# Optimization experiments

Hardware: AMD Instinct MI355X
Metric: run time of the kernel (lower is better)

The kernel has to match this reference:

```python
import jax, jax.numpy as jnp
import numpy as np

N, K, FN, O = 2048, 8, 16, 32


def setup_inputs() -> dict:
    key = jax.random.key(0)
    k1, k2, k3, k4 = jax.random.split(key, 4)
    node_features = jax.random.normal(k1, (N, FN), dtype=jnp.float32)
    edge_feat_matrix = jax.random.normal(k2, (N, N, K), dtype=jnp.float32)
    adj_matrix = jax.random.uniform(k3, (N, N), dtype=jnp.float32)
    stdv = 1.0 / np.sqrt(O)
    weight = jax.random.uniform(k4, (K + FN, O), dtype=jnp.float32,
                                minval=-stdv, maxval=stdv)
    return {"node_features": node_features,
            "edge_feat_matrix": edge_feat_matrix,
            "adj_matrix": adj_matrix,
            "weight": weight}


def reference(node_features, edge_feat_matrix, adj_matrix, weight):
    # Row-normalize adjacency: D^{-1} A (tensor_normalize in __init__)
    row_sum = adj_matrix.sum(axis=1)
    r_inv = jnp.where(jnp.isfinite(1.0 / row_sum), 1.0 / row_sum, 0.0)
    adj = r_inv[:, None] * adj_matrix  # [N, N]

    # Original math: combined[i,j] = cat(edge[i,j], x[j]); support = combined @ W
    # out[j,o] = sum_i adj[i,j] * support[i,j,o]
    # Split W so we never materialize the [N,N,K+FN] or [N,N,O] tensors.
    k = edge_feat_matrix.shape[-1]
    W_e, W_n = weight[:k], weight[k:]
    agg_e = jnp.einsum('ij,ijk->jk', adj, edge_feat_matrix)  # [N, K]
    col_sum = adj.sum(axis=0)                                 # [N]
    out = agg_e @ W_e + col_sum[:, None] * (node_features @ W_n)  # [N, O]
    return out
```

## Files before the change

### kernel.cpp

```cpp
#include <hip/hip_runtime.h>
#include <hip/hip_bf16.h>

constexpr int CN  = 2048;
constexpr int CK  = 8;
constexpr int CFN = 16;
constexpr int CO  = 32;

constexpr int JTILE  = 256;
constexpr int NJT    = CN / JTILE;
constexpr int CHUNK  = 32;
constexpr int NCHUNK = CN / CHUNK;

__global__ __launch_bounds__(256) void rowsum_k(const float* __restrict__ adj,
                                                float* __restrict__ rinv) {
    const int i = blockIdx.x;
    const int t = threadIdx.x;
    const float4* row = (const float4*)(adj + (size_t)i * CN);
    float4 v0 = row[t], v1 = row[t + 256];
    float s = v0.x + v0.y + v0.z + v0.w + v1.x + v1.y + v1.z + v1.w;
    #pragma unroll
    for (int off = 32; off > 0; off >>= 1) s += __shfl_down(s, off, 64);
    __shared__ float partial[4];
    if ((t & 63) == 0) partial[t >> 6] = s;
    __syncthreads();
    if (t == 0) {
        float tot = partial[0] + partial[1] + partial[2] + partial[3];
        float r = 1.0f / tot;
        if (!isfinite(r)) r = 0.0f;
        rinv[i] = r;
    }
}

__global__ __launch_bounds__(256) void main_k(const float* __restrict__ E,
                                              const float* __restrict__ adj,
                                              const float* __restrict__ rinv,
                                              float* __restrict__ agg,
                                              float* __restrict__ col) {
    const int j  = blockIdx.x * JTILE + threadIdx.x;
    const int i0 = blockIdx.y * CHUNK;

    float acc[CK];
    #pragma unroll
    for (int k = 0; k < CK; ++k) acc[k] = 0.f;
    float colacc = 0.f;

    #pragma unroll 4
    for (int ii = 0; ii < CHUNK; ++ii) {
        const int i = i0 + ii;
        const float a = rinv[i] * adj[(size_t)i * CN + j];
        const float4* ev = (const float4*)(E + ((size_t)i * CN + j) * CK);
        const float4 e0 = ev[0];
        const float4 e1 = ev[1];
        acc[0] += a * e0.x; acc[1] += a * e0.y;
        acc[2] += a * e0.z; acc[3] += a * e0.w;
        acc[4] += a * e1.x; acc[5] += a * e1.y;
        acc[6] += a * e1.z; acc[7] += a * e1.w;
        colacc += a;
    }

    float* aj = agg + (size_t)j * CK;
    #pragma unroll
    for (int k = 0; k < CK; ++k) atomicAdd(aj + k, acc[k]);
    atomicAdd(col + j, colacc);
}

__global__ __launch_bounds__(256) void epilogue_k(const float* __restrict__ agg,
                                                  const float* __restrict__ col,
                                                  const float* __restrict__ nf,
                                                  const float* __restrict__ wt,
                                                  float* __restrict__ out) {
    const int gid = blockIdx.x * 256 + threadIdx.x;
    const int j = gid >> 5;
    const int o = gid & 31;
    float s1 = 0.f;
    #pragma unroll
    for (int k = 0; k < CK; ++k)
        s1 += agg[(size_t)j * CK + k] * wt[k * CO + o];
    float s2 = 0.f;
    #pragma unroll
    for (int f = 0; f < CFN; ++f)
        s2 += nf[(size_t)j * CFN + f] * wt[(CK + f) * CO + o];
    out[gid] = s1 + col[j] * s2;
}

extern "C" void kernel_launch(void* const* d_in, const int* in_sizes, int n_in,
                              void* d_out, int out_size, void* d_ws, size_t ws_size,
                              hipStream_t stream) {
    const float *nf = nullptr, *E = nullptr, *adj = nullptr, *wt = nullptr;
    for (int i = 0; i < n_in; ++i) {
        switch (in_sizes[i]) {
            case CN * CFN:        nf  = (const float*)d_in[i]; break;
            case CN * CN * CK:    E   = (const float*)d_in[i]; break;
            case CN * CN:         adj = (const float*)d_in[i]; break;
            case (CK + CFN) * CO: wt  = (const float*)d_in[i]; break;
        }
    }
    float* out = (float*)d_out;

    float* rinv = (float*)d_ws;
    float* agg  = rinv + CN;
    float* col  = agg + (size_t)CN * CK;
    size_t zero_bytes = (size_t)(CN + CN * CK + CN) * sizeof(float);
    hipMemsetAsync(d_ws, 0, zero_bytes, stream);

    rowsum_k<<<CN, 256, 0, stream>>>(adj, rinv);
    main_k<<<dim3(NJT, NCHUNK), 256, 0, stream>>>(E, adj, rinv, agg, col);
    epilogue_k<<<(CN * CO) / 256, 256, 0, stream>>>(agg, col, nf, wt, out);
}
```

Measured before the change: 230.3 us.

## Replace global atomics with per-chunk partial buffers and a separate reduce kernel

The main kernel now writes each chunk's nine accumulators (eight edge sums plus the column sum) into a partial buffer laid out k-major, with no atomic adds. A new reduce kernel sums the 64 chunk partials for each (k, j), and the epilogue reads the transposed result. This drops the memset and the atomic contention on agg and col. In exchange it adds one kernel launch and about 4.7 MB of partial-buffer writes and reads.

```diff
diff --git a/kernel.cpp b/kernel.cpp
--- a/kernel.cpp
+++ b/kernel.cpp
@@ -10,6 +10,7 @@
 constexpr int NJT    = CN / JTILE;
 constexpr int CHUNK  = 32;
 constexpr int NCHUNK = CN / CHUNK;
+constexpr int NACC   = CK + 1;
 
 __global__ __launch_bounds__(256) void rowsum_k(const float* __restrict__ adj,
                                                 float* __restrict__ rinv) {
@@ -34,15 +35,15 @@
 __global__ __launch_bounds__(256) void main_k(const float* __restrict__ E,
                                               const float* __restrict__ adj,
                                               const float* __restrict__ rinv,
-                                              float* __restrict__ agg,
-                                              float* __restrict__ col) {
-    const int j  = blockIdx.x * JTILE + threadIdx.x;
-    const int i0 = blockIdx.y * CHUNK;
+                                              float* __restrict__ part) {
+    const int t  = threadIdx.x;
+    const int j  = blockIdx.x * JTILE + t;
+    const int ic = blockIdx.y;
+    const int i0 = ic * CHUNK;
 
-    float acc[CK];
+    float acc[NACC];
     #pragma unroll
-    for (int k = 0; k < CK; ++k) acc[k] = 0.f;
-    float colacc = 0.f;
+    for (int k = 0; k < NACC; ++k) acc[k] = 0.f;
 
     #pragma unroll 4
     for (int ii = 0; ii < CHUNK; ++ii) {
@@ -55,17 +56,27 @@
         acc[2] += a * e0.z; acc[3] += a * e0.w;
         acc[4] += a * e1.x; acc[5] += a * e1.y;
         acc[6] += a * e1.z; acc[7] += a * e1.w;
-        colacc += a;
+        acc[8] += a;
     }
 
-    float* aj = agg + (size_t)j * CK;
     #pragma unroll
-    for (int k = 0; k < CK; ++k) atomicAdd(aj + k, acc[k]);
-    atomicAdd(col + j, colacc);
+    for (int k = 0; k < NACC; ++k)
+        part[(size_t)k * (NCHUNK * CN) + (size_t)ic * CN + j] = acc[k];
 }
 
-__global__ __launch_bounds__(256) void epilogue_k(const float* __restrict__ agg,
-                                                  const float* __restrict__ col,
+__global__ __launch_bounds__(256) void reduce_k(const float* __restrict__ part,
+                                                float* __restrict__ aggT) {
+    const int gid = blockIdx.x * 256 + threadIdx.x;
+    const int k = gid >> 11;
+    const int j = gid & (CN - 1);
+    const float* p = part + (size_t)k * (NCHUNK * CN) + j;
+    float s = 0.f;
+    #pragma unroll 8
+    for (int ic = 0; ic < NCHUNK; ++ic) s += p[(size_t)ic * CN];
+    aggT[gid] = s;
+}
+
+__global__ __launch_bounds__(256) void epilogue_k(const float* __restrict__ aggT,
                                                   const float* __restrict__ nf,
                                                   const float* __restrict__ wt,
                                                   float* __restrict__ out) {
@@ -75,12 +86,12 @@
     float s1 = 0.f;
     #pragma unroll
     for (int k = 0; k < CK; ++k)
-        s1 += agg[(size_t)j * CK + k] * wt[k * CO + o];
+        s1 += aggT[(size_t)k * CN + j] * wt[k * CO + o];
     float s2 = 0.f;
     #pragma unroll
     for (int f = 0; f < CFN; ++f)
         s2 += nf[(size_t)j * CFN + f] * wt[(CK + f) * CO + o];
-    out[gid] = s1 + col[j] * s2;
+    out[gid] = s1 + aggT[(size_t)CK * CN + j] * s2;
 }
 
 extern "C" void kernel_launch(void* const* d_in, const int* in_sizes, int n_in,
@@ -98,12 +109,11 @@
     float* out = (float*)d_out;
 
     float* rinv = (float*)d_ws;
-    float* agg  = rinv + CN;
-    float* col  = agg + (size_t)CN * CK;
-    size_t zero_bytes = (size_t)(CN + CN * CK + CN) * sizeof(float);
-    hipMemsetAsync(d_ws, 0, zero_bytes, stream);
+    float* part = rinv + CN;
+    float* aggT = part + (size_t)NACC * NCHUNK * CN;
 
     rowsum_k<<<CN, 256, 0, stream>>>(adj, rinv);
-    main_k<<<dim3(NJT, NCHUNK), 256, 0, stream>>>(E, adj, rinv, agg, col);
-    epilogue_k<<<(CN * CO) / 256, 256, 0, stream>>>(agg, col, nf, wt, out);
+    main_k<<<dim3(NJT, NCHUNK), 256, 0, stream>>>(E, adj, rinv, part);
+    reduce_k<<<(NACC * CN) / 256, 256, 0, stream>>>(part, aggT);
+    epilogue_k<<<(CN * CO) / 256, 256, 0, stream>>>(aggT, nf, wt, out);
 }
```

After: 215.2 us. 6.5% less time.
